# Kernel optimization log

Hardware: AMD Instinct MI355X
Metric: run time of the kernel (lower is better)

## Reference

```python
import jax, jax.numpy as jnp
import numpy as np

D_MODEL = 1024
NUM_HEADS = 16
DEPTH = D_MODEL // NUM_HEADS  # 64
BATCH, SEQ = 4, 2048


def setup_inputs() -> dict:
    key = jax.random.key(0)
    ks = jax.random.split(key, 9)
    s = 1.0 / np.sqrt(D_MODEL)
    x = jax.random.normal(ks[0], (BATCH, SEQ, D_MODEL), dtype=jnp.float32)
    # Per-head Dense weights stacked on a leading head axis [H, d_model, depth]
    Wq = jax.random.normal(ks[1], (NUM_HEADS, D_MODEL, DEPTH), dtype=jnp.float32) * s
    Wk = jax.random.normal(ks[2], (NUM_HEADS, D_MODEL, DEPTH), dtype=jnp.float32) * s
    Wv = jax.random.normal(ks[3], (NUM_HEADS, D_MODEL, DEPTH), dtype=jnp.float32) * s
    bq = jnp.zeros((NUM_HEADS, DEPTH), dtype=jnp.float32)
    bk = jnp.zeros((NUM_HEADS, DEPTH), dtype=jnp.float32)
    bv = jnp.zeros((NUM_HEADS, DEPTH), dtype=jnp.float32)
    Wo = jax.random.normal(ks[4], (D_MODEL, D_MODEL), dtype=jnp.float32) * s
    bo = jnp.zeros((D_MODEL,), dtype=jnp.float32)
    return {"x": x, "Wq": Wq, "bq": bq, "Wk": Wk, "bk": bk,
            "Wv": Wv, "bv": bv, "Wo": Wo, "bo": bo}


def reference(x, Wq, bq, Wk, bk, Wv, bv, Wo, bo):
    # Batched equivalent of the per-head loop: project, attend, concat heads.
    q = jnp.einsum('bsd,hde->bhse', x, Wq) + bq[:, None, :]  # [B,H,S,depth]
    k = jnp.einsum('bsd,hde->bhse', x, Wk) + bk[:, None, :]
    v = jnp.einsum('bsd,hde->bhse', x, Wv) + bv[:, None, :]
    scale = 1.0 / jnp.sqrt(jnp.asarray(DEPTH, dtype=x.dtype))
    scores = jnp.einsum('bhse,bhte->bhst', q, k) * scale      # [B,H,S,S]
    weights = jax.nn.softmax(scores, axis=-1)
    heads = jnp.einsum('bhst,bhte->bhse', weights, v)         # [B,H,S,depth]
    # concat head outputs along last axis in head order (tf.concat axis=-1)
    multi = jnp.transpose(heads, (0, 2, 1, 3)).reshape(x.shape[0], x.shape[1], D_MODEL)
    return multi @ Wo + bo
```

## Files before the change

### kernel.cpp

```cpp
#include <hip/hip_runtime.h>
#include <hip/hip_bf16.h>

#define BATCH 4
#define SEQ   2048
#define DM    1024
#define NH    16
#define DEPTH 64
#define ROWS  (BATCH*SEQ)
#define NQKV  (3*DM)
#define BH    (BATCH*NH)

typedef __attribute__((ext_vector_type(8))) short bf16x8;
typedef __attribute__((ext_vector_type(4))) float f32x4;
typedef __attribute__((ext_vector_type(16))) float f32x16;
typedef unsigned short u16;
typedef unsigned int   u32;

__device__ __forceinline__ u16 f2bf(float f) {
    union { float f; unsigned u; } v; v.f = f;
    unsigned r = v.u + 0x7fff + ((v.u >> 16) & 1);
    return (u16)(r >> 16);
}

__device__ __forceinline__ u32 pk2bf(float a, float b) {
#if __has_builtin(__builtin_amdgcn_cvt_pk_bf16_f32)
    typedef __attribute__((ext_vector_type(2))) __bf16 v2bf;
    union { v2bf v; u32 u; } u_;
    u_.v = __builtin_amdgcn_cvt_pk_bf16_f32(a, b);
    return u_.u;
#else
    return (u32)f2bf(a) | ((u32)f2bf(b) << 16);
#endif
}

__device__ __forceinline__ void pl32swap(u32& x, u32& y) {
#if __has_builtin(__builtin_amdgcn_permlane32_swap)
    typedef __attribute__((ext_vector_type(2))) int v2i;
    v2i r = __builtin_amdgcn_permlane32_swap((int)x, (int)y, false, false);
    x = (u32)r[0]; y = (u32)r[1];
#else
    u32 sx = (u32)__shfl_xor((int)x, 32);
    u32 sy = (u32)__shfl_xor((int)y, 32);
    bool hi = (threadIdx.x & 32) != 0;
    u32 nx = hi ? sy : x;
    u32 ny = hi ? y : sx;
    x = nx; y = ny;
#endif
}

__device__ __forceinline__ bf16x8 pack4(u32 a, u32 b, u32 c, u32 d) {
    union { u32 u[4]; bf16x8 v; } x;
    x.u[0] = a; x.u[1] = b; x.u[2] = c; x.u[3] = d;
    return x.v;
}

__device__ __forceinline__ void g2l16(void* lds, const void* g) {
    __builtin_amdgcn_global_load_lds((const __attribute__((address_space(1))) void*)g,
                                     (__attribute__((address_space(3))) void*)lds, 16, 0, 0);
}

__device__ __forceinline__ bf16x8 frag8(const u16* tile, int row, int gl) {
    return *(const bf16x8*)(tile + row * 64 + ((gl ^ (row & 7)) * 8));
}

__device__ __forceinline__ f32x16 mfma32(bf16x8 a, bf16x8 b, f32x16 c) {
    return __builtin_amdgcn_mfma_f32_32x32x16_bf16(a, b, c, 0, 0, 0);
}

__global__ __launch_bounds__(256) void k_prep(const float* __restrict__ x,
                                              const float* __restrict__ Wq, const float* __restrict__ Wk,
                                              const float* __restrict__ Wv, const float* __restrict__ Wo,
                                              u16* __restrict__ xb, u16* __restrict__ BT, u16* __restrict__ WoT) {
    __shared__ u16 T[64][65];
    int tid = threadIdx.x;
    int bx = blockIdx.x;
    if (bx < 2048) {
        int i = bx * 4096 + tid * 4;
        for (int l = 0; l < 4; ++l) {
            float4 v = *(const float4*)(x + i + l * 1024);
            ushort4 o; o.x = f2bf(v.x); o.y = f2bf(v.y); o.z = f2bf(v.z); o.w = f2bf(v.w);
            *(ushort4*)(xb + i + l * 1024) = o;
        }
        return;
    }
    if (bx < 2816) {
        int q = bx - 2048;
        int kt = q & 15, mh = q >> 4, m = mh >> 4, h = mh & 15;
        const float* W = (m == 0) ? Wq : (m == 1) ? Wk : Wv;
        const float* src = W + ((size_t)h * 1024 + kt * 64) * 64;
        int e = tid & 63, r0 = tid >> 6;
        for (int i = 0; i < 16; ++i) { int r = i * 4 + r0; T[r][e] = f2bf(src[r * 64 + e]); }
        __syncthreads();
        int kk = tid & 63, e0 = tid >> 6;
        u16* dst = BT + ((size_t)m * 1024 + h * 64) * 1024 + kt * 64;
        for (int i = 0; i < 16; ++i) { int ee = i * 4 + e0; dst[ee * 1024 + kk] = T[kk][ee]; }
        return;
    }
    {
        int q = bx - 2816;
        int kt = q & 15, nt = q >> 4;
        const float* src = Wo + (size_t)kt * 64 * 1024 + nt * 64;
        int c = tid & 63, r0 = tid >> 6;
        for (int i = 0; i < 16; ++i) { int r = i * 4 + r0; T[r][c] = f2bf(src[r * 1024 + c]); }
        __syncthreads();
        int kk = tid & 63, e0 = tid >> 6;
        u16* dst = WoT + (size_t)nt * 64 * 1024 + kt * 64;
        for (int i = 0; i < 16; ++i) { int ee = i * 4 + e0; dst[ee * 1024 + kk] = T[kk][ee]; }
    }
}

__global__ __launch_bounds__(256) void k_gemm_qkv(const u16* __restrict__ xb, const u16* __restrict__ Wt,
                                                  const float* __restrict__ bq, const float* __restrict__ bk,
                                                  const float* __restrict__ bv,
                                                  u16* __restrict__ Q, u16* __restrict__ K, u16* __restrict__ VT) {
    __shared__ u16 Al[128 * 64];
    __shared__ u16 Bl[128 * 64];
    int tid = threadIdx.x;
    int wave = tid >> 6, lane = tid & 63, ln = lane & 15, quad = lane >> 4;
    int b = blockIdx.x;
    bool isvt = (b >= 1024);
    int row0, col0;
    const u16 *Am, *Bm;
    if (!isvt) {
        col0 = (b & 15) * 128; row0 = (b >> 4) * 128;
        Am = xb + (size_t)row0 * 1024; Bm = Wt + (size_t)col0 * 1024;
    } else {
        int b2 = b - 1024;
        col0 = (b2 & 63) * 128; row0 = (b2 >> 6) * 128;
        Am = Wt + (size_t)2048 * 1024 + (size_t)row0 * 1024; Bm = xb + (size_t)col0 * 1024;
    }
    int moff = (wave >> 1) * 64, noff = (wave & 1) * 64;
    f32x4 acc[4][4] = {};

    for (int k0 = 0; k0 < 1024; k0 += 64) {
        for (int l = 0; l < 4; ++l) {
            int idx = tid + l * 256, r = idx >> 3, gs = ((idx & 7) ^ (r & 7)) * 8;
            g2l16(&Al[idx * 8], Am + r * 1024 + k0 + gs);
            g2l16(&Bl[idx * 8], Bm + r * 1024 + k0 + gs);
        }
        __syncthreads();
        for (int kk = 0; kk < 2; ++kk) {
            bf16x8 a[4], bb[4];
            for (int i = 0; i < 4; ++i) a[i]  = frag8(Al, moff + i * 16 + ln, kk * 4 + quad);
            for (int j = 0; j < 4; ++j) bb[j] = frag8(Bl, noff + j * 16 + ln, kk * 4 + quad);
            for (int i = 0; i < 4; ++i)
                for (int j = 0; j < 4; ++j)
                    acc[i][j] = __builtin_amdgcn_mfma_f32_16x16x32_bf16(a[i], bb[j], acc[i][j], 0, 0, 0);
        }
        __syncthreads();
    }

    if (!isvt) {
        const float QSCALE = 0.125f * 1.4426950408889634f;
        for (int j = 0; j < 4; ++j) {
            int c = col0 + noff + j * 16 + ln;
            int m = c >> 10, h = (c >> 6) & 15, e = c & 63;
            const float* bias = (m == 0) ? bq : bk;
            float bval = bias[h * 64 + e];
            for (int i = 0; i < 4; ++i)
                for (int r = 0; r < 4; ++r) {
                    int rowg = row0 + moff + i * 16 + quad * 4 + r;
                    int b_ = rowg >> 11, s = rowg & 2047;
                    int bh = b_ * 16 + h;
                    float v = acc[i][j][r] + bval;
                    if (m == 0) Q[(bh * 2048 + s) * 64 + e] = f2bf(v * QSCALE);
                    else        K[(bh * 2048 + s) * 64 + e] = f2bf(v);
                }
        }
    } else {
        for (int j = 0; j < 4; ++j) {
            int c = col0 + noff + j * 16 + ln;
            int b_ = c >> 11, s = c & 2047;
            for (int i = 0; i < 4; ++i)
                for (int r = 0; r < 4; ++r) {
                    int ii = row0 + moff + i * 16 + quad * 4 + r;
                    float v = acc[i][j][r] + bv[ii];
                    VT[((size_t)b_ * 1024 + ii) * 2048 + s] = f2bf(v);
                }
        }
    }
}

__global__ __launch_bounds__(256, 2) void k_attn(const u16* __restrict__ Q, const u16* __restrict__ K,
                                                 const u16* __restrict__ VT, u16* __restrict__ A2) {
    __shared__ u16 Vl[2][64 * 64];
    __shared__ float linv[256];
    int tid = threadIdx.x;
    int w = tid >> 6, lane = tid & 63, l31 = lane & 31, h = lane >> 5;
    int bh = blockIdx.y;
    int m0 = blockIdx.x * 256;
    const u16* Qb = Q + (size_t)bh * 2048 * 64;
    const u16* Kb = K + (size_t)bh * 2048 * 64;
    const u16* Vb = VT + (size_t)bh * 64 * 2048;

    int sidx[2]; const u16* vsrc[2];
    for (int rr = 0; rr < 2; ++rr) {
        int idx = tid + rr * 256, r = idx >> 3, g = (idx & 7) ^ (r & 7);
        sidx[rr] = idx * 8;
        vsrc[rr] = Vb + r * 2048 + g * 8;
    }
    g2l16(&Vl[0][sidx[0]], vsrc[0]);
    g2l16(&Vl[0][sidx[1]], vsrc[1]);

    bf16x8 qb[2][4];
    for (int qt = 0; qt < 2; ++qt)
        for (int s = 0; s < 4; ++s)
            qb[qt][s] = *(const bf16x8*)(Qb + (m0 + w * 64 + qt * 32 + l31) * 64 + s * 16 + h * 8);
    __syncthreads();

    f32x16 oacc[2][2] = {};
    float lsum[2] = {0.f, 0.f};

    for (int t = 0; t < 32; ++t) {
        const u16* Kt = Kb + t * 64 * 64;
        bf16x8 kf[2][4];
        for (int kt = 0; kt < 2; ++kt)
            for (int s = 0; s < 4; ++s)
                kf[kt][s] = *(const bf16x8*)(Kt + (kt * 32 + l31) * 64 + s * 16 + h * 8);

        if (t < 31) {
            g2l16(&Vl[(t + 1) & 1][sidx[0]], vsrc[0] + (t + 1) * 64);
            g2l16(&Vl[(t + 1) & 1][sidx[1]], vsrc[1] + (t + 1) * 64);
        }
        const u16* vb = Vl[t & 1];

        for (int kt = 0; kt < 2; ++kt) {
            f32x16 sc[2] = {};
            for (int s = 0; s < 4; ++s) {
                sc[0] = mfma32(kf[kt][s], qb[0][s], sc[0]);
                sc[1] = mfma32(kf[kt][s], qb[1][s], sc[1]);
            }
            bf16x8 vf00 = frag8(vb, l31,      kt * 4 + h);
            bf16x8 vf01 = frag8(vb, l31,      kt * 4 + 2 + h);
            bf16x8 vf10 = frag8(vb, 32 + l31, kt * 4 + h);
            bf16x8 vf11 = frag8(vb, 32 + l31, kt * 4 + 2 + h);
            for (int qt = 0; qt < 2; ++qt) {
                u32 g[8]; float sq = 0.f;
                for (int gi = 0; gi < 8; ++gi) {
                    float p0 = __builtin_amdgcn_exp2f(sc[qt][2 * gi]);
                    float p1 = __builtin_amdgcn_exp2f(sc[qt][2 * gi + 1]);
                    sq += p0 + p1;
                    g[gi] = pk2bf(p0, p1);
                }
                lsum[qt] += sq;
                pl32swap(g[0], g[2]); pl32swap(g[1], g[3]);
                pl32swap(g[4], g[6]); pl32swap(g[5], g[7]);
                bf16x8 a0 = pack4(g[0], g[1], g[2], g[3]);
                bf16x8 a1 = pack4(g[4], g[5], g[6], g[7]);
                oacc[qt][0] = mfma32(a0, vf00, oacc[qt][0]);
                oacc[qt][0] = mfma32(a1, vf01, oacc[qt][0]);
                oacc[qt][1] = mfma32(a0, vf10, oacc[qt][1]);
                oacc[qt][1] = mfma32(a1, vf11, oacc[qt][1]);
            }
        }
        __syncthreads();
    }

    for (int qt = 0; qt < 2; ++qt) {
        float l2 = lsum[qt] + __shfl_xor(lsum[qt], 32);
        linv[w * 64 + qt * 32 + l31] = 1.0f / l2;
    }
    int b_ = bh >> 4, hh = bh & 15;
    for (int qt = 0; qt < 2; ++qt)
        for (int g = 0; g < 4; ++g) {
            f32x4 iv = *(f32x4*)&linv[w * 64 + qt * 32 + 8 * g + 4 * h];
            for (int dt = 0; dt < 2; ++dt)
                for (int r = 0; r < 4; ++r) {
                    int row = b_ * 2048 + m0 + w * 64 + qt * 32 + 8 * g + 4 * h + r;
                    A2[row * 1024 + hh * 64 + dt * 32 + l31] = f2bf(oacc[qt][dt][g * 4 + r] * iv[r]);
                }
        }
}

__global__ __launch_bounds__(256) void k_gemm_out(const u16* __restrict__ A, const u16* __restrict__ BT,
                                                  const float* __restrict__ bo, float* __restrict__ out) {
    __shared__ u16 Al[128 * 64];
    __shared__ u16 Bl[128 * 64];
    int tid = threadIdx.x;
    int wave = tid >> 6, lane = tid & 63, ln = lane & 15, quad = lane >> 4;
    int row0 = blockIdx.y * 128;
    int col0 = blockIdx.x * 128;
    int moff = (wave >> 1) * 64, noff = (wave & 1) * 64;
    f32x4 acc[4][4] = {};

    for (int k0 = 0; k0 < 1024; k0 += 64) {
        for (int l = 0; l < 4; ++l) {
            int idx = tid + l * 256, r = idx >> 3, gs = ((idx & 7) ^ (r & 7)) * 8;
            g2l16(&Al[idx * 8], A  + (row0 + r) * 1024 + k0 + gs);
            g2l16(&Bl[idx * 8], BT + (col0 + r) * 1024 + k0 + gs);
        }
        __syncthreads();
        for (int kk = 0; kk < 2; ++kk) {
            bf16x8 a[4], b[4];
            for (int i = 0; i < 4; ++i) a[i] = frag8(Al, moff + i * 16 + ln, kk * 4 + quad);
            for (int j = 0; j < 4; ++j) b[j] = frag8(Bl, noff + j * 16 + ln, kk * 4 + quad);
            for (int i = 0; i < 4; ++i)
                for (int j = 0; j < 4; ++j)
                    acc[i][j] = __builtin_amdgcn_mfma_f32_16x16x32_bf16(a[i], b[j], acc[i][j], 0, 0, 0);
        }
        __syncthreads();
    }

    for (int j = 0; j < 4; ++j) {
        int c = col0 + noff + j * 16 + ln;
        float bias = bo[c];
        for (int i = 0; i < 4; ++i)
            for (int r = 0; r < 4; ++r) {
                int rowg = row0 + moff + i * 16 + quad * 4 + r;
                out[rowg * 1024 + c] = acc[i][j][r] + bias;
            }
    }
}

extern "C" void kernel_launch(void* const* d_in, const int* in_sizes, int n_in,
                              void* d_out, int out_size, void* d_ws, size_t ws_size,
                              hipStream_t stream) {
    const float* x  = (const float*)d_in[0];
    const float* Wq = (const float*)d_in[1];
    const float* bq = (const float*)d_in[2];
    const float* Wk = (const float*)d_in[3];
    const float* bk = (const float*)d_in[4];
    const float* Wv = (const float*)d_in[5];
    const float* bv = (const float*)d_in[6];
    const float* Wo = (const float*)d_in[7];
    const float* bo = (const float*)d_in[8];
    float* out = (float*)d_out;

    char* ws = (char*)d_ws;
    u16* xb    = (u16*)ws; ws += (size_t)ROWS * DM * 2;
    u16* WqkvT = (u16*)ws; ws += (size_t)NQKV * DM * 2;
    u16* WoT   = (u16*)ws; ws += (size_t)DM * DM * 2;
    u16* Qb    = (u16*)ws; ws += (size_t)BH * SEQ * DEPTH * 2;
    u16* Kb    = (u16*)ws; ws += (size_t)BH * SEQ * DEPTH * 2;
    u16* VTb   = (u16*)ws; ws += (size_t)BH * SEQ * DEPTH * 2;
    u16* A2    = (u16*)ws; ws += (size_t)ROWS * DM * 2;

    k_prep     <<<dim3(3072),   dim3(256), 0, stream>>>(x, Wq, Wk, Wv, Wo, xb, WqkvT, WoT);
    k_gemm_qkv <<<dim3(1536),   dim3(256), 0, stream>>>(xb, WqkvT, bq, bk, bv, Qb, Kb, VTb);
    k_attn     <<<dim3(8, 64),  dim3(256), 0, stream>>>(Qb, Kb, VTb, A2);
    k_gemm_out <<<dim3(8, 64),  dim3(256), 0, stream>>>(A2, WoT, bo, out);
}
```

Baseline: 302.9 us.

## Load V fragments directly from global and prefetch K in registers in attention

```diff
diff --git a/kernel.cpp b/kernel.cpp
--- a/kernel.cpp
+++ b/kernel.cpp
@@ -183,62 +183,58 @@
 
 __global__ __launch_bounds__(256, 2) void k_attn(const u16* __restrict__ Q, const u16* __restrict__ K,
                                                  const u16* __restrict__ VT, u16* __restrict__ A2) {
-    __shared__ u16 Vl[2][64 * 64];
     __shared__ float linv[256];
     int tid = threadIdx.x;
     int w = tid >> 6, lane = tid & 63, l31 = lane & 31, h = lane >> 5;
-    int bh = blockIdx.y;
-    int m0 = blockIdx.x * 256;
+    int bh = blockIdx.x;
+    int m0 = blockIdx.y * 256;
     const u16* Qb = Q + (size_t)bh * 2048 * 64;
     const u16* Kb = K + (size_t)bh * 2048 * 64;
     const u16* Vb = VT + (size_t)bh * 64 * 2048;
-
-    int sidx[2]; const u16* vsrc[2];
-    for (int rr = 0; rr < 2; ++rr) {
-        int idx = tid + rr * 256, r = idx >> 3, g = (idx & 7) ^ (r & 7);
-        sidx[rr] = idx * 8;
-        vsrc[rr] = Vb + r * 2048 + g * 8;
-    }
-    g2l16(&Vl[0][sidx[0]], vsrc[0]);
-    g2l16(&Vl[0][sidx[1]], vsrc[1]);
 
     bf16x8 qb[2][4];
     for (int qt = 0; qt < 2; ++qt)
         for (int s = 0; s < 4; ++s)
             qb[qt][s] = *(const bf16x8*)(Qb + (m0 + w * 64 + qt * 32 + l31) * 64 + s * 16 + h * 8);
-    __syncthreads();
+
+    const u16* kbase  = Kb + l31 * 64 + h * 8;
+    const u16* vbase0 = Vb + (size_t)l31 * 2048 + h * 8;
+    const u16* vbase1 = Vb + (size_t)(32 + l31) * 2048 + h * 8;
+
+    bf16x8 kf[2][4];
+    for (int kt = 0; kt < 2; ++kt)
+        for (int s = 0; s < 4; ++s)
+            kf[kt][s] = *(const bf16x8*)(kbase + kt * 2048 + s * 16);
 
     f32x16 oacc[2][2] = {};
     float lsum[2] = {0.f, 0.f};
 
     for (int t = 0; t < 32; ++t) {
-        const u16* Kt = Kb + t * 64 * 64;
-        bf16x8 kf[2][4];
+        bf16x8 vf[2][2][2];
         for (int kt = 0; kt < 2; ++kt)
-            for (int s = 0; s < 4; ++s)
-                kf[kt][s] = *(const bf16x8*)(Kt + (kt * 32 + l31) * 64 + s * 16 + h * 8);
-
-        if (t < 31) {
-            g2l16(&Vl[(t + 1) & 1][sidx[0]], vsrc[0] + (t + 1) * 64);
-            g2l16(&Vl[(t + 1) & 1][sidx[1]], vsrc[1] + (t + 1) * 64);
-        }
-        const u16* vb = Vl[t & 1];
-
-        for (int kt = 0; kt < 2; ++kt) {
-            f32x16 sc[2] = {};
-            for (int s = 0; s < 4; ++s) {
-                sc[0] = mfma32(kf[kt][s], qb[0][s], sc[0]);
-                sc[1] = mfma32(kf[kt][s], qb[1][s], sc[1]);
+            for (int u = 0; u < 2; ++u) {
+                vf[kt][0][u] = *(const bf16x8*)(vbase0 + t * 64 + kt * 32 + u * 16);
+                vf[kt][1][u] = *(const bf16x8*)(vbase1 + t * 64 + kt * 32 + u * 16);
             }
-            bf16x8 vf00 = frag8(vb, l31,      kt * 4 + h);
-            bf16x8 vf01 = frag8(vb, l31,      kt * 4 + 2 + h);
-            bf16x8 vf10 = frag8(vb, 32 + l31, kt * 4 + h);
-            bf16x8 vf11 = frag8(vb, 32 + l31, kt * 4 + 2 + h);
+
+        f32x16 sc[2][2] = {};
+        for (int s = 0; s < 4; ++s)
+            for (int kt = 0; kt < 2; ++kt) {
+                sc[kt][0] = mfma32(kf[kt][s], qb[0][s], sc[kt][0]);
+                sc[kt][1] = mfma32(kf[kt][s], qb[1][s], sc[kt][1]);
+            }
+
+        if (t < 31)
+            for (int kt = 0; kt < 2; ++kt)
+                for (int s = 0; s < 4; ++s)
+                    kf[kt][s] = *(const bf16x8*)(kbase + (t + 1) * 4096 + kt * 2048 + s * 16);
+
+        for (int kt = 0; kt < 2; ++kt)
             for (int qt = 0; qt < 2; ++qt) {
                 u32 g[8]; float sq = 0.f;
                 for (int gi = 0; gi < 8; ++gi) {
-                    float p0 = __builtin_amdgcn_exp2f(sc[qt][2 * gi]);
-                    float p1 = __builtin_amdgcn_exp2f(sc[qt][2 * gi + 1]);
+                    float p0 = __builtin_amdgcn_exp2f(sc[kt][qt][2 * gi]);
+                    float p1 = __builtin_amdgcn_exp2f(sc[kt][qt][2 * gi + 1]);
                     sq += p0 + p1;
                     g[gi] = pk2bf(p0, p1);
                 }
@@ -247,13 +243,11 @@
                 pl32swap(g[4], g[6]); pl32swap(g[5], g[7]);
                 bf16x8 a0 = pack4(g[0], g[1], g[2], g[3]);
                 bf16x8 a1 = pack4(g[4], g[5], g[6], g[7]);
-                oacc[qt][0] = mfma32(a0, vf00, oacc[qt][0]);
-                oacc[qt][0] = mfma32(a1, vf01, oacc[qt][0]);
-                oacc[qt][1] = mfma32(a0, vf10, oacc[qt][1]);
-                oacc[qt][1] = mfma32(a1, vf11, oacc[qt][1]);
+                oacc[qt][0] = mfma32(a0, vf[kt][0][0], oacc[qt][0]);
+                oacc[qt][0] = mfma32(a1, vf[kt][0][1], oacc[qt][0]);
+                oacc[qt][1] = mfma32(a0, vf[kt][1][0], oacc[qt][1]);
+                oacc[qt][1] = mfma32(a1, vf[kt][1][1], oacc[qt][1]);
             }
-        }
-        __syncthreads();
     }
 
     for (int qt = 0; qt < 2; ++qt) {
@@ -337,6 +331,6 @@
 
     k_prep     <<<dim3(3072),   dim3(256), 0, stream>>>(x, Wq, Wk, Wv, Wo, xb, WqkvT, WoT);
     k_gemm_qkv <<<dim3(1536),   dim3(256), 0, stream>>>(xb, WqkvT, bq, bk, bv, Qb, Kb, VTb);
-    k_attn     <<<dim3(8, 64),  dim3(256), 0, stream>>>(Qb, Kb, VTb, A2);
+    k_attn     <<<dim3(64, 8),  dim3(256), 0, stream>>>(Qb, Kb, VTb, A2);
     k_gemm_out <<<dim3(8, 64),  dim3(256), 0, stream>>>(A2, WoT, bo, out);
 }
```

New measurement: 329.0 us. 8.6% more time.
